# Performance work log

Measured on AMD Instinct MI355X. Metric: run time of the kernel, lower is better.

Reference implementation:

```python
import jax, jax.numpy as jnp
import numpy as np

IN_SIZE = 512
NUM_ACTIONS = 32
ACTION_DIM = 64
INNER_DIM = 1024
HIDDEN_DIM = 512
N_LAYERS = 2
B, S = 8, 4096


def setup_inputs() -> dict:
    key = jax.random.key(0)
    ks = jax.random.split(key, 16)
    H, D = HIDDEN_DIM, INNER_DIM
    inp = {
        "batch_world_states_tensor": jax.random.normal(ks[0], (B, S, IN_SIZE), dtype=jnp.float32),
        "batch_action_indices": jax.random.randint(ks[1], (B, S), 0, NUM_ACTIONS, dtype=jnp.int64),
        # action embedding table
        "emb": jax.random.normal(ks[2], (NUM_ACTIONS, ACTION_DIM), dtype=jnp.float32),
        # in_proj Linear(in_size -> inner_dim - action_dim)
        "Wp": jax.random.normal(ks[3], (D - ACTION_DIM, IN_SIZE), dtype=jnp.float32) * 0.03,
        "bp": jax.random.uniform(ks[4], (D - ACTION_DIM,), minval=-0.005, maxval=0.005, dtype=jnp.float32),
        # LSTM layer 0 (input dim = inner_dim)
        "Wih0": jax.random.normal(ks[5], (4 * H, D), dtype=jnp.float32) * 0.03,
        "Whh0": jax.random.normal(ks[6], (4 * H, H), dtype=jnp.float32) * 0.03,
        "bih0": jax.random.uniform(ks[7], (4 * H,), minval=-0.005, maxval=0.005, dtype=jnp.float32),
        "bhh0": jax.random.uniform(ks[8], (4 * H,), minval=-0.005, maxval=0.005, dtype=jnp.float32),
        # LSTM layer 1 (input dim = hidden_dim)
        "Wih1": jax.random.normal(ks[9], (4 * H, H), dtype=jnp.float32) * 0.03,
        "Whh1": jax.random.normal(ks[10], (4 * H, H), dtype=jnp.float32) * 0.03,
        "bih1": jax.random.uniform(ks[11], (4 * H,), minval=-0.005, maxval=0.005, dtype=jnp.float32),
        "bhh1": jax.random.uniform(ks[12], (4 * H,), minval=-0.005, maxval=0.005, dtype=jnp.float32),
    }
    return inp


def _lstm_cell(x, h, c, Wih, Whh, b):
    # x: [B, Din], h/c: [B, H]; PyTorch gate order: i, f, g, o
    gates = x @ Wih.T + h @ Whh.T + b  # [B, 4H]
    i, f, g, o = jnp.split(gates, 4, axis=-1)
    c_new = jax.nn.sigmoid(f) * c + jax.nn.sigmoid(i) * jnp.tanh(g)
    h_new = jax.nn.sigmoid(o) * jnp.tanh(c_new)
    return h_new, c_new


def reference(batch_world_states_tensor, batch_action_indices, emb, Wp, bp,
              Wih0, Whh0, bih0, bhh0, Wih1, Whh1, bih1, bhh1):
    # embed actions + project world states, concat -> [B, S, inner_dim]
    act = emb[batch_action_indices]                              # [B,S,action_dim]
    proj = jax.nn.relu(jnp.einsum('bsi,oi->bso', batch_world_states_tensor, Wp) + bp)
    x = jnp.concatenate([proj, act], axis=-1)                    # [B,S,inner_dim]

    b0 = bih0 + bhh0
    b1 = bih1 + bhh1
    Bsz = x.shape[0]
    H = Whh0.shape[1]
    h0 = jnp.zeros((Bsz, H), dtype=x.dtype)
    init = (h0, h0, h0, h0)  # (h_l0, c_l0, h_l1, c_l1)

    def step(carry, x_t):
        h_0, c_0, h_1, c_1 = carry
        h_0, c_0 = _lstm_cell(x_t, h_0, c_0, Wih0, Whh0, b0)
        h_1, c_1 = _lstm_cell(h_0, h_1, c_1, Wih1, Whh1, b1)
        return (h_0, c_0, h_1, c_1), h_1

    xs = jnp.swapaxes(x, 0, 1)                                   # [S,B,inner]
    (h_0, c_0, h_1, c_1), out = jax.lax.scan(step, init, xs)
    rnn_out = jnp.swapaxes(out, 0, 1)                            # [B,S,H]
    hidden = jnp.stack([h_0, h_1], axis=0)                       # [L,B,H]
    cell = jnp.stack([c_0, c_1], axis=0)
    return rnn_out, (hidden, cell)
```

## Files before the change

kernel.cpp:

```cpp
#include <hip/hip_runtime.h>

typedef _Float16 f16;
typedef __attribute__((ext_vector_type(4))) _Float16 f16x4;
typedef __attribute__((ext_vector_type(8))) _Float16 f16x8;
typedef __attribute__((ext_vector_type(4))) float f32x4;

#define NB 8
#define NS 4096
#define NIN 512
#define NDIN 1024
#define NH 512
#define NG4 2048
#define NPROJ 960

static const size_t OFF_XH  = 0;
static const size_t OFF_GX  = (size_t)NB*NS*NDIN*2;
static const size_t OFF_H0  = OFF_GX + (size_t)NB*NS*NG4*2;
static const size_t OFF_H1  = OFF_H0 + 32768;
static const size_t OFF_CNT = OFF_H1 + 32768;

__device__ __forceinline__ float sigf(float x)  { return 1.f/(1.f+__expf(-x)); }
__device__ __forceinline__ float tanh_(float x) { return 2.f/(1.f+__expf(-2.f*x)) - 1.f; }

__device__ __forceinline__ f16x8 cvt8(const float* p) {
  float4 a = *(const float4*)p;
  float4 b = *(const float4*)(p+4);
  f16x8 r = {(f16)a.x,(f16)a.y,(f16)a.z,(f16)a.w,(f16)b.x,(f16)b.y,(f16)b.z,(f16)b.w};
  return r;
}

__global__ void init_kernel(unsigned* __restrict__ p, int n) {
  int i = blockIdx.x*blockDim.x + threadIdx.x;
  for (; i < n; i += gridDim.x*blockDim.x) p[i] = 0u;
}

__global__ void emb_kernel(const int* __restrict__ idx, const float* __restrict__ emb,
                           f16* __restrict__ xh) {
  int g  = blockIdx.x*blockDim.x + threadIdx.x;
  int bt = g >> 4;
  int j  = (g & 15) << 2;
  int id = idx[bt];
  float4 v = *(const float4*)(emb + id*64 + j);
  f16x4 h = {(f16)v.x,(f16)v.y,(f16)v.z,(f16)v.w};
  *(f16x4*)(xh + (size_t)bt*NDIN + NPROJ + j) = h;
}

__global__ __launch_bounds__(256) void proj_kernel(
    const float* __restrict__ wst, const float* __restrict__ Wp,
    const float* __restrict__ bp, f16* __restrict__ xh) {
  __shared__ f16 Asl[128*40];
  __shared__ f16 Bsl[128*40];
  const int tid = threadIdx.x;
  const int lane = tid & 63;
  const int wv = tid >> 6;
  const int wm = wv >> 1, wn = wv & 1;
  const int lm = lane & 15;
  const int kq = lane >> 4;
  const int kg8 = kq << 3;
  const int m0 = blockIdx.x * 128;
  const int n0 = blockIdx.y * 128;
  f32x4 acc[4][4];
#pragma unroll
  for (int a = 0; a < 4; ++a)
#pragma unroll
    for (int b = 0; b < 4; ++b) acc[a][b] = (f32x4){0.f,0.f,0.f,0.f};
  for (int k0 = 0; k0 < NIN; k0 += 32) {
#pragma unroll
    for (int i = 0; i < 4; ++i) {
      int c = tid + (i << 8);
      int row = c >> 3;
      int kc = (c & 7) << 2;
      {
        float4 v = *(const float4*)(wst + (size_t)(m0+row)*NIN + k0 + kc);
        f16x4 h = {(f16)v.x,(f16)v.y,(f16)v.z,(f16)v.w};
        *(f16x4*)&Asl[row*40 + kc] = h;
      }
      {
        int nr = n0 + row; nr = nr < NPROJ ? nr : (NPROJ-1);
        float4 v = *(const float4*)(Wp + (size_t)nr*NIN + k0 + kc);
        f16x4 h = {(f16)v.x,(f16)v.y,(f16)v.z,(f16)v.w};
        *(f16x4*)&Bsl[row*40 + kc] = h;
      }
    }
    __syncthreads();
    f16x8 af[4], bf[4];
#pragma unroll
    for (int f = 0; f < 4; ++f) af[f] = *(f16x8*)&Asl[(wm*64 + f*16 + lm)*40 + kg8];
#pragma unroll
    for (int f = 0; f < 4; ++f) bf[f] = *(f16x8*)&Bsl[(wn*64 + f*16 + lm)*40 + kg8];
#pragma unroll
    for (int a = 0; a < 4; ++a)
#pragma unroll
      for (int b = 0; b < 4; ++b)
        acc[a][b] = __builtin_amdgcn_mfma_f32_16x16x32_f16(af[a], bf[b], acc[a][b], 0,0,0);
    __syncthreads();
  }
#pragma unroll
  for (int a = 0; a < 4; ++a)
#pragma unroll
    for (int b = 0; b < 4; ++b) {
      int n = n0 + wn*64 + b*16 + lm;
      if (n < NPROJ) {
        float bias = bp[n];
#pragma unroll
        for (int j = 0; j < 4; ++j) {
          int m = m0 + wm*64 + a*16 + (kq<<2) + j;
          float v = acc[a][b][j] + bias;
          xh[(size_t)m*NDIN + n] = (f16)fmaxf(v, 0.f);
        }
      }
    }
}

__global__ __launch_bounds__(256) void gx_kernel(
    const f16* __restrict__ xh, const float* __restrict__ Wih0,
    const float* __restrict__ bih0, const float* __restrict__ bhh0,
    f16* __restrict__ gx) {
  __shared__ f16 Asl[128*40];
  __shared__ f16 Bsl[128*40];
  const int tid = threadIdx.x;
  const int lane = tid & 63;
  const int wv = tid >> 6;
  const int wm = wv >> 1, wn = wv & 1;
  const int lm = lane & 15;
  const int kq = lane >> 4;
  const int kg8 = kq << 3;
  const int m0 = blockIdx.x * 128;
  const int n0 = blockIdx.y * 128;
  f32x4 acc[4][4];
#pragma unroll
  for (int a = 0; a < 4; ++a)
#pragma unroll
    for (int b = 0; b < 4; ++b) acc[a][b] = (f32x4){0.f,0.f,0.f,0.f};
  for (int k0 = 0; k0 < NDIN; k0 += 32) {
#pragma unroll
    for (int i = 0; i < 2; ++i) {
      int c = tid + (i << 8);
      int row = c >> 2;
      int kc = (c & 3) << 3;
      f16x8 v = *(const f16x8*)(xh + (size_t)(m0+row)*NDIN + k0 + kc);
      *(f16x8*)&Asl[row*40 + kc] = v;
    }
#pragma unroll
    for (int i = 0; i < 4; ++i) {
      int c = tid + (i << 8);
      int row = c >> 3;
      int kc = (c & 7) << 2;
      int n = n0 + row;
      int orig = ((n & 3) << 9) | (n >> 2);
      float4 v = *(const float4*)(Wih0 + (size_t)orig*NDIN + k0 + kc);
      f16x4 h = {(f16)v.x,(f16)v.y,(f16)v.z,(f16)v.w};
      *(f16x4*)&Bsl[row*40 + kc] = h;
    }
    __syncthreads();
    f16x8 af[4], bf[4];
#pragma unroll
    for (int f = 0; f < 4; ++f) af[f] = *(f16x8*)&Asl[(wm*64 + f*16 + lm)*40 + kg8];
#pragma unroll
    for (int f = 0; f < 4; ++f) bf[f] = *(f16x8*)&Bsl[(wn*64 + f*16 + lm)*40 + kg8];
#pragma unroll
    for (int a = 0; a < 4; ++a)
#pragma unroll
      for (int b = 0; b < 4; ++b)
        acc[a][b] = __builtin_amdgcn_mfma_f32_16x16x32_f16(af[a], bf[b], acc[a][b], 0,0,0);
    __syncthreads();
  }
#pragma unroll
  for (int a = 0; a < 4; ++a)
#pragma unroll
    for (int b = 0; b < 4; ++b) {
      int n = n0 + wn*64 + b*16 + lm;
      int orig = ((n & 3) << 9) | (n >> 2);
      float bias = bih0[orig] + bhh0[orig];
#pragma unroll
      for (int j = 0; j < 4; ++j) {
        int m = m0 + wm*64 + a*16 + (kq<<2) + j;
        gx[(size_t)m*NG4 + n] = (f16)(acc[a][b][j] + bias);
      }
    }
}

__global__ __launch_bounds__(512, 2) void seq_kernel(
    const f16* __restrict__ gx, const float* __restrict__ Whh0,
    const float* __restrict__ Wih1, const float* __restrict__ Whh1,
    const float* __restrict__ bih1, const float* __restrict__ bhh1,
    f16* __restrict__ h0b, f16* __restrict__ h1b,
    unsigned* __restrict__ cnt, float* __restrict__ out) {
  const int tid  = threadIdx.x;
  const int lane = tid & 63;
  const int w    = (blockIdx.x << 3) + (tid >> 6);
  const bool isG0 = (w < 128);
  const int rt = isG0 ? w : (w - 128);
  const int lm  = lane & 15;
  const int kq  = lane >> 4;
  const int kg8 = kq << 3;
  const int prow = (rt << 4) + lm;
  const int orig = ((prow & 3) << 9) | (prow >> 2);
  const int u    = (rt << 2) + kq;
  const int bb   = (lm < 8) ? lm : 0;
  const bool act = (lm < 8);

  f16x8 wA[16], wB[16];
  if (isG0) {
    const float* s = Whh0 + (size_t)orig * NH;
#pragma unroll
    for (int kt = 0; kt < 16; ++kt) wA[kt] = cvt8(s + kt*32 + kg8);
#pragma unroll
    for (int kt = 0; kt < 16; ++kt) wB[kt] = wA[kt];
  } else {
    const float* s1 = Wih1 + (size_t)orig * NH;
    const float* s2 = Whh1 + (size_t)orig * NH;
#pragma unroll
    for (int kt = 0; kt < 16; ++kt) wA[kt] = cvt8(s1 + kt*32 + kg8);
#pragma unroll
    for (int kt = 0; kt < 16; ++kt) wB[kt] = cvt8(s2 + kt*32 + kg8);
  }
  float bias1_[4] = {0.f,0.f,0.f,0.f};
  if (!isG0) {
#pragma unroll
    for (int j = 0; j < 4; ++j) bias1_[j] = bih1[j*NH + u] + bhh1[j*NH + u];
  }

  float cst = 0.f, hlast = 0.f;
  const unsigned nwg = gridDim.x;

  for (int p = 0; p <= NS; ++p) {
    const int qr = (p + 1) & 1;
    const int qw = p & 1;
    if (isG0) {
      if (p < NS) {
        f16x4 g4 = *(const f16x4*)(gx + ((size_t)bb*NS + p)*NG4 + (u << 2));
        const f16* hp = h0b + qr*8192 + (lm << 9);
        f32x4 acc = (f32x4){0.f,0.f,0.f,0.f};
#pragma unroll
        for (int kt = 0; kt < 16; ++kt) {
          f16x8 bfr = *(const f16x8*)(hp + kt*32 + kg8);
          acc = __builtin_amdgcn_mfma_f32_16x16x32_f16(wA[kt], bfr, acc, 0,0,0);
        }
        float gi = acc[0] + (float)g4[0];
        float gf = acc[1] + (float)g4[1];
        float gg = acc[2] + (float)g4[2];
        float go = acc[3] + (float)g4[3];
        cst = sigf(gf)*cst + sigf(gi)*tanh_(gg);
        float h = sigf(go)*tanh_(cst);
        hlast = h;
        if (act) h0b[qw*8192 + (lm << 9) + u] = (f16)h;
      }
    } else {
      if (p >= 1) {
        const f16* hp0 = h0b + qr*8192 + (lm << 9);
        const f16* hp1 = h1b + qw*8192 + (lm << 9);
        f32x4 acc = (f32x4){0.f,0.f,0.f,0.f};
#pragma unroll
        for (int kt = 0; kt < 16; ++kt) {
          f16x8 bfr = *(const f16x8*)(hp0 + kt*32 + kg8);
          acc = __builtin_amdgcn_mfma_f32_16x16x32_f16(wA[kt], bfr, acc, 0,0,0);
        }
#pragma unroll
        for (int kt = 0; kt < 16; ++kt) {
          f16x8 bfr = *(const f16x8*)(hp1 + kt*32 + kg8);
          acc = __builtin_amdgcn_mfma_f32_16x16x32_f16(wB[kt], bfr, acc, 0,0,0);
        }
        float gi = acc[0] + bias1_[0];
        float gf = acc[1] + bias1_[1];
        float gg = acc[2] + bias1_[2];
        float go = acc[3] + bias1_[3];
        cst = sigf(gf)*cst + sigf(gi)*tanh_(gg);
        float h = sigf(go)*tanh_(cst);
        hlast = h;
        if (act) {
          h1b[qr*8192 + (lm << 9) + u] = (f16)h;
          out[((size_t)lm*NS + (p-1))*NH + u] = h;
        }
      }
    }
    __syncthreads();
    if (tid == 0) {
      __hip_atomic_fetch_add(cnt, 1u, __ATOMIC_RELEASE, __HIP_MEMORY_SCOPE_AGENT);
      const unsigned tgt = nwg * (unsigned)(p + 1);
      while (__hip_atomic_load(cnt, __ATOMIC_ACQUIRE, __HIP_MEMORY_SCOPE_AGENT) < tgt) {
        __builtin_amdgcn_s_sleep(1);
      }
    }
    __syncthreads();
  }

  if (act) {
    const size_t HID = (size_t)NB*NS*NH;
    size_t base = (size_t)lm*NH + u;
    if (isG0) {
      out[HID + base] = hlast;
      out[HID + 8192 + base] = cst;
    } else {
      out[HID + 4096 + base] = hlast;
      out[HID + 8192 + 4096 + base] = cst;
    }
  }
}

extern "C" void kernel_launch(void* const* d_in, const int* in_sizes, int n_in,
                              void* d_out, int out_size, void* d_ws, size_t ws_size,
                              hipStream_t stream) {
  const float* wst  = (const float*)d_in[0];
  const int*   idx  = (const int*)  d_in[1];
  const float* emb  = (const float*)d_in[2];
  const float* Wp   = (const float*)d_in[3];
  const float* bp   = (const float*)d_in[4];
  const float* Wih0 = (const float*)d_in[5];
  const float* Whh0 = (const float*)d_in[6];
  const float* bih0 = (const float*)d_in[7];
  const float* bhh0 = (const float*)d_in[8];
  const float* Wih1 = (const float*)d_in[9];
  const float* Whh1 = (const float*)d_in[10];
  const float* bih1 = (const float*)d_in[11];
  const float* bhh1 = (const float*)d_in[12];
  float* out = (float*)d_out;
  char* wsb = (char*)d_ws;
  f16* xh  = (f16*)(wsb + OFF_XH);
  f16* gx  = (f16*)(wsb + OFF_GX);
  f16* h0b = (f16*)(wsb + OFF_H0);
  f16* h1b = (f16*)(wsb + OFF_H1);
  unsigned* cnt = (unsigned*)(wsb + OFF_CNT);

  hipLaunchKernelGGL(init_kernel, dim3(32), dim3(256), 0, stream,
                     (unsigned*)(wsb + OFF_H0), (int)((32768 + 32768 + 256) / 4));
  hipLaunchKernelGGL(proj_kernel, dim3(256, 8), dim3(256), 0, stream, wst, Wp, bp, xh);
  hipLaunchKernelGGL(emb_kernel, dim3(2048), dim3(256), 0, stream, idx, emb, xh);
  hipLaunchKernelGGL(gx_kernel, dim3(256, 16), dim3(256), 0, stream, xh, Wih0, bih0, bhh0, gx);
  hipLaunchKernelGGL(seq_kernel, dim3(32), dim3(512), 0, stream,
                     gx, Whh0, Wih1, Whh1, bih1, bhh1, h0b, h1b, cnt, out);
}
```

Measured before the change: 40.72 ms.

## Replace atomic-counter grid barrier with per-block flag array and coherent stores

Swaps the single atomic counter grid barrier for a flag-array barrier. Each workgroup writes its own step flag, and one wavefront polls all 32 flags with cache-bypassing loads. Hidden-state stores use sc0 sc1 coherent stores followed by an explicit vmcnt drain. The layer-0 branch also prefetches the next step's gx values and splits the MFMA chain into two accumulators for more ILP, and each branch is specialised by block index. The intent is to cut per-step barrier latency from atomic contention, at the cost of relying on inline-asm cache bits for correctness.

```diff
diff --git a/kernel.cpp b/kernel.cpp
--- a/kernel.cpp
+++ b/kernel.cpp
@@ -17,7 +17,7 @@
 static const size_t OFF_GX  = (size_t)NB*NS*NDIN*2;
 static const size_t OFF_H0  = OFF_GX + (size_t)NB*NS*NG4*2;
 static const size_t OFF_H1  = OFF_H0 + 32768;
-static const size_t OFF_CNT = OFF_H1 + 32768;
+static const size_t OFF_ARR = OFF_H1 + 32768;
 
 __device__ __forceinline__ float sigf(float x)  { return 1.f/(1.f+__expf(-x)); }
 __device__ __forceinline__ float tanh_(float x) { return 2.f/(1.f+__expf(-2.f*x)) - 1.f; }
@@ -27,6 +27,36 @@
   float4 b = *(const float4*)(p+4);
   f16x8 r = {(f16)a.x,(f16)a.y,(f16)a.z,(f16)a.w,(f16)b.x,(f16)b.y,(f16)b.z,(f16)b.w};
   return r;
+}
+
+__device__ __forceinline__ void st_h_coh(f16* p, float h) {
+  f16 hf = (f16)h;
+  unsigned short hv = *(unsigned short*)&hf;
+  asm volatile("global_store_short %0, %1, off sc0 sc1" :: "v"(p), "v"(hv) : "memory");
+}
+__device__ __forceinline__ void st_flag(unsigned* p, unsigned v) {
+  asm volatile("global_store_dword %0, %1, off sc0 sc1" :: "v"(p), "v"(v) : "memory");
+}
+__device__ __forceinline__ unsigned ld_flag(const unsigned* p) {
+  unsigned v;
+  asm volatile("global_load_dword %0, %1, off sc0 sc1\n\ts_waitcnt vmcnt(0)"
+               : "=v"(v) : "v"(p) : "memory");
+  return v;
+}
+__device__ __forceinline__ void drain_vm() {
+  asm volatile("s_waitcnt vmcnt(0)" ::: "memory");
+}
+
+__device__ __forceinline__ void phase_barrier(unsigned* arr, int wg, unsigned tgt) {
+  __syncthreads();
+  if (threadIdx.x < 64) {
+    if (threadIdx.x == 0) st_flag(arr + wg, tgt);
+    const unsigned* ap = arr + (threadIdx.x & 31);
+    unsigned v;
+    do { v = ld_flag(ap); } while (!__all((int)(v >= tgt)));
+    __builtin_amdgcn_fence(__ATOMIC_ACQUIRE, "agent");
+  }
+  __syncthreads();
 }
 
 __global__ void init_kernel(unsigned* __restrict__ p, int n) {
@@ -185,113 +215,121 @@
     const float* __restrict__ Wih1, const float* __restrict__ Whh1,
     const float* __restrict__ bih1, const float* __restrict__ bhh1,
     f16* __restrict__ h0b, f16* __restrict__ h1b,
-    unsigned* __restrict__ cnt, float* __restrict__ out) {
+    unsigned* __restrict__ arr, float* __restrict__ out) {
   const int tid  = threadIdx.x;
   const int lane = tid & 63;
-  const int w    = (blockIdx.x << 3) + (tid >> 6);
-  const bool isG0 = (w < 128);
-  const int rt = isG0 ? w : (w - 128);
   const int lm  = lane & 15;
   const int kq  = lane >> 4;
   const int kg8 = kq << 3;
-  const int prow = (rt << 4) + lm;
-  const int orig = ((prow & 3) << 9) | (prow >> 2);
-  const int u    = (rt << 2) + kq;
-  const int bb   = (lm < 8) ? lm : 0;
-  const bool act = (lm < 8);
-
-  f16x8 wA[16], wB[16];
-  if (isG0) {
-    const float* s = Whh0 + (size_t)orig * NH;
-#pragma unroll
-    for (int kt = 0; kt < 16; ++kt) wA[kt] = cvt8(s + kt*32 + kg8);
-#pragma unroll
-    for (int kt = 0; kt < 16; ++kt) wB[kt] = wA[kt];
-  } else {
-    const float* s1 = Wih1 + (size_t)orig * NH;
-    const float* s2 = Whh1 + (size_t)orig * NH;
-#pragma unroll
-    for (int kt = 0; kt < 16; ++kt) wA[kt] = cvt8(s1 + kt*32 + kg8);
-#pragma unroll
-    for (int kt = 0; kt < 16; ++kt) wB[kt] = cvt8(s2 + kt*32 + kg8);
-  }
-  float bias1_[4] = {0.f,0.f,0.f,0.f};
-  if (!isG0) {
-#pragma unroll
-    for (int j = 0; j < 4; ++j) bias1_[j] = bih1[j*NH + u] + bhh1[j*NH + u];
-  }
-
-  float cst = 0.f, hlast = 0.f;
-  const unsigned nwg = gridDim.x;
-
-  for (int p = 0; p <= NS; ++p) {
-    const int qr = (p + 1) & 1;
-    const int qw = p & 1;
-    if (isG0) {
-      if (p < NS) {
-        f16x4 g4 = *(const f16x4*)(gx + ((size_t)bb*NS + p)*NG4 + (u << 2));
-        const f16* hp = h0b + qr*8192 + (lm << 9);
-        f32x4 acc = (f32x4){0.f,0.f,0.f,0.f};
-#pragma unroll
-        for (int kt = 0; kt < 16; ++kt) {
-          f16x8 bfr = *(const f16x8*)(hp + kt*32 + kg8);
-          acc = __builtin_amdgcn_mfma_f32_16x16x32_f16(wA[kt], bfr, acc, 0,0,0);
-        }
-        float gi = acc[0] + (float)g4[0];
-        float gf = acc[1] + (float)g4[1];
-        float gg = acc[2] + (float)g4[2];
-        float go = acc[3] + (float)g4[3];
-        cst = sigf(gf)*cst + sigf(gi)*tanh_(gg);
-        float h = sigf(go)*tanh_(cst);
-        hlast = h;
-        if (act) h0b[qw*8192 + (lm << 9) + u] = (f16)h;
-      }
-    } else {
-      if (p >= 1) {
-        const f16* hp0 = h0b + qr*8192 + (lm << 9);
-        const f16* hp1 = h1b + qw*8192 + (lm << 9);
-        f32x4 acc = (f32x4){0.f,0.f,0.f,0.f};
-#pragma unroll
-        for (int kt = 0; kt < 16; ++kt) {
-          f16x8 bfr = *(const f16x8*)(hp0 + kt*32 + kg8);
-          acc = __builtin_amdgcn_mfma_f32_16x16x32_f16(wA[kt], bfr, acc, 0,0,0);
-        }
-#pragma unroll
-        for (int kt = 0; kt < 16; ++kt) {
-          f16x8 bfr = *(const f16x8*)(hp1 + kt*32 + kg8);
-          acc = __builtin_amdgcn_mfma_f32_16x16x32_f16(wB[kt], bfr, acc, 0,0,0);
-        }
-        float gi = acc[0] + bias1_[0];
-        float gf = acc[1] + bias1_[1];
-        float gg = acc[2] + bias1_[2];
-        float go = acc[3] + bias1_[3];
-        cst = sigf(gf)*cst + sigf(gi)*tanh_(gg);
-        float h = sigf(go)*tanh_(cst);
-        hlast = h;
-        if (act) {
-          h1b[qr*8192 + (lm << 9) + u] = (f16)h;
-          out[((size_t)lm*NS + (p-1))*NH + u] = h;
-        }
-      }
-    }
-    __syncthreads();
-    if (tid == 0) {
-      __hip_atomic_fetch_add(cnt, 1u, __ATOMIC_RELEASE, __HIP_MEMORY_SCOPE_AGENT);
-      const unsigned tgt = nwg * (unsigned)(p + 1);
-      while (__hip_atomic_load(cnt, __ATOMIC_ACQUIRE, __HIP_MEMORY_SCOPE_AGENT) < tgt) {
-        __builtin_amdgcn_s_sleep(1);
-      }
-    }
-    __syncthreads();
-  }
-
-  if (act) {
-    const size_t HID = (size_t)NB*NS*NH;
-    size_t base = (size_t)lm*NH + u;
-    if (isG0) {
+  const size_t HID = (size_t)NB*NS*NH;
+
+  if (blockIdx.x < 16) {
+    const int rt = (blockIdx.x << 3) + (tid >> 6);
+    const int prow = (rt << 4) + lm;
+    const int orig = ((prow & 3) << 9) | (prow >> 2);
+    const int u    = (rt << 2) + kq;
+    const int bb   = (lm < 8) ? lm : 0;
+    const bool act = (lm < 8);
+
+    f16x8 wA[16];
+    {
+      const float* s = Whh0 + (size_t)orig * NH;
+#pragma unroll
+      for (int kt = 0; kt < 16; ++kt) wA[kt] = cvt8(s + kt*32 + kg8);
+#pragma unroll
+      for (int kt = 0; kt < 16; ++kt) asm volatile("" : "+v"(wA[kt]));
+    }
+
+    float cst = 0.f, hlast = 0.f;
+    f16x4 gcur = *(const f16x4*)(gx + ((size_t)bb*NS)*NG4 + (u << 2));
+
+    for (int k = 0; k < NS; ++k) {
+      f16x4 gnxt = gcur;
+      if (k + 1 < NS)
+        gnxt = *(const f16x4*)(gx + ((size_t)bb*NS + (k+1))*NG4 + (u << 2));
+      const f16* hp = h0b + ((k+1)&1)*8192 + (lm << 9);
+      f32x4 a0 = (f32x4){0.f,0.f,0.f,0.f}, a1 = (f32x4){0.f,0.f,0.f,0.f};
+#pragma unroll
+      for (int kt = 0; kt < 16; kt += 2) {
+        a0 = __builtin_amdgcn_mfma_f32_16x16x32_f16(wA[kt],   *(const f16x8*)(hp + kt*32 + kg8),      a0, 0,0,0);
+        a1 = __builtin_amdgcn_mfma_f32_16x16x32_f16(wA[kt+1], *(const f16x8*)(hp + kt*32 + 32 + kg8), a1, 0,0,0);
+      }
+      float gi = a0[0] + a1[0] + (float)gcur[0];
+      float gf = a0[1] + a1[1] + (float)gcur[1];
+      float gg = a0[2] + a1[2] + (float)gcur[2];
+      float go = a0[3] + a1[3] + (float)gcur[3];
+      cst = sigf(gf)*cst + sigf(gi)*tanh_(gg);
+      float h = sigf(go)*tanh_(cst);
+      hlast = h;
+      if (act) st_h_coh(h0b + (k&1)*8192 + (lm << 9) + u, h);
+      drain_vm();
+      gcur = gnxt;
+      phase_barrier(arr, blockIdx.x, (unsigned)(k+1));
+    }
+    if (act) {
+      size_t base = (size_t)lm*NH + u;
       out[HID + base] = hlast;
       out[HID + 8192 + base] = cst;
-    } else {
+    }
+  } else {
+    const int rt = ((blockIdx.x - 16) << 3) + (tid >> 6);
+    const int prow = (rt << 4) + lm;
+    const int orig = ((prow & 3) << 9) | (prow >> 2);
+    const int u    = (rt << 2) + kq;
+    const bool act = (lm < 8);
+
+    f16x8 wA[16], wB[16];
+    {
+      const float* s1 = Wih1 + (size_t)orig * NH;
+      const float* s2 = Whh1 + (size_t)orig * NH;
+#pragma unroll
+      for (int kt = 0; kt < 16; ++kt) wA[kt] = cvt8(s1 + kt*32 + kg8);
+#pragma unroll
+      for (int kt = 0; kt < 16; ++kt) wB[kt] = cvt8(s2 + kt*32 + kg8);
+#pragma unroll
+      for (int kt = 0; kt < 16; ++kt) {
+        asm volatile("" : "+v"(wA[kt]));
+        asm volatile("" : "+v"(wB[kt]));
+      }
+    }
+    float bias1_[4];
+#pragma unroll
+    for (int j = 0; j < 4; ++j) bias1_[j] = bih1[j*NH + u] + bhh1[j*NH + u];
+
+    float cst = 0.f, hlast = 0.f;
+
+    auto g1_step = [&](int k, bool final_) {
+      const f16* hp0 = h0b + ((k+1)&1)*8192 + (lm << 9);
+      const f16* hp1 = h1b + (k&1)*8192 + (lm << 9);
+      f32x4 a0 = (f32x4){0.f,0.f,0.f,0.f}, a1 = (f32x4){0.f,0.f,0.f,0.f};
+#pragma unroll
+      for (int kt = 0; kt < 16; ++kt)
+        a0 = __builtin_amdgcn_mfma_f32_16x16x32_f16(wA[kt], *(const f16x8*)(hp0 + kt*32 + kg8), a0, 0,0,0);
+#pragma unroll
+      for (int kt = 0; kt < 16; ++kt)
+        a1 = __builtin_amdgcn_mfma_f32_16x16x32_f16(wB[kt], *(const f16x8*)(hp1 + kt*32 + kg8), a1, 0,0,0);
+      float gi = a0[0] + a1[0] + bias1_[0];
+      float gf = a0[1] + a1[1] + bias1_[1];
+      float gg = a0[2] + a1[2] + bias1_[2];
+      float go = a0[3] + a1[3] + bias1_[3];
+      cst = sigf(gf)*cst + sigf(gi)*tanh_(gg);
+      float h = sigf(go)*tanh_(cst);
+      hlast = h;
+      if (act) {
+        if (!final_) st_h_coh(h1b + ((k+1)&1)*8192 + (lm << 9) + u, h);
+        out[((size_t)lm*NS + (k-1))*NH + u] = h;
+      }
+    };
+
+    for (int k = 0; k < NS; ++k) {
+      if (k >= 1) g1_step(k, false);
+      drain_vm();
+      phase_barrier(arr, blockIdx.x, (unsigned)(k+1));
+    }
+    g1_step(NS, true);
+
+    if (act) {
+      size_t base = (size_t)lm*NH + u;
       out[HID + 4096 + base] = hlast;
       out[HID + 8192 + 4096 + base] = cst;
     }
@@ -320,7 +358,7 @@
   f16* gx  = (f16*)(wsb + OFF_GX);
   f16* h0b = (f16*)(wsb + OFF_H0);
   f16* h1b = (f16*)(wsb + OFF_H1);
-  unsigned* cnt = (unsigned*)(wsb + OFF_CNT);
+  unsigned* arr = (unsigned*)(wsb + OFF_ARR);
 
   hipLaunchKernelGGL(init_kernel, dim3(32), dim3(256), 0, stream,
                      (unsigned*)(wsb + OFF_H0), (int)((32768 + 32768 + 256) / 4));
@@ -328,5 +366,5 @@
   hipLaunchKernelGGL(emb_kernel, dim3(2048), dim3(256), 0, stream, idx, emb, xh);
   hipLaunchKernelGGL(gx_kernel, dim3(256, 16), dim3(256), 0, stream, xh, Wih0, bih0, bhh0, gx);
   hipLaunchKernelGGL(seq_kernel, dim3(32), dim3(512), 0, stream,
-                     gx, Whh0, Wih1, Whh1, bih1, bhh1, h0b, h1b, cnt, out);
-}
+                     gx, Whh0, Wih1, Whh1, bih1, bhh1, h0b, h1b, arr, out);
+}
```

Measured after the change: 37.93 ms. -6.9%, faster.
